# Performance work log

Measured on AMD Instinct MI355X. Metric: run time of the kernel, lower is better.

Reference implementation:

```python
import jax, jax.numpy as jnp
import numpy as np

THRESH = 0.3

def _quantize_ternary(s):
    # straight-through ternary: forward value is q, gradient is identity
    q = jnp.where(s > THRESH, 1.0, jnp.where(s < -THRESH, -1.0, 0.0))
    return s + jax.lax.stop_gradient(q - s)

def setup_inputs() -> dict:
    key = jax.random.key(0)
    k1, k2, k3 = jax.random.split(key, 3)
    B, D, T, C = 32768, 1024, 16, 1000
    x = jax.random.normal(k1, (B, D), dtype=jnp.float32)
    sigs_raw = jax.random.normal(k2, (T, D), dtype=jnp.float32) * 0.5
    # per-tile Linear(d_model, n_classes): weight [C, D], bias [C]
    W = jax.random.normal(k3, (T, C, D), dtype=jnp.float32) / np.sqrt(D)
    b = jnp.zeros((T, C), dtype=jnp.float32)
    return {"x": x, "sigs_raw": sigs_raw, "W": W, "b": b}

def reference(x, sigs_raw, W, b):
    sigs = _quantize_ternary(sigs_raw)          # [T, D] ternary values
    scores = x @ sigs.T                          # [B, T]
    tile_indices = jnp.argmax(scores, axis=-1)   # [B] top-1 routing
    n_tiles = W.shape[0]
    logits = jnp.zeros((x.shape[0], W.shape[1]), dtype=x.dtype)  # [B, C]
    # static loop over tiles: masked per-expert linear, combined by select
    for t in range(n_tiles):
        m = (tile_indices == t)[:, None]         # [B, 1]
        yt = x @ W[t].T + b[t]                   # [B, C]
        logits = jnp.where(m, yt, logits)
    return logits, tile_indices
```

## Files before the change

kernel.cpp:

```cpp
#include <hip/hip_runtime.h>

#define NBROWS 32768
#define ND 1024
#define NT 16
#define NC 1000
#define NHB 128
#define MAX_RB128 272

typedef short short8 __attribute__((ext_vector_type(8)));
typedef float f32x4 __attribute__((ext_vector_type(4)));
typedef unsigned short ushort_t;

typedef __attribute__((address_space(1))) const unsigned int* gas_t;
typedef __attribute__((address_space(3))) unsigned int* las_t;

__device__ __forceinline__ void async_copy16(const void* g, void* l) {
  __builtin_amdgcn_global_load_lds((gas_t)g, (las_t)l, 16, 0, 0);
}

__device__ __forceinline__ unsigned f2bf(float f) {
  unsigned u = __float_as_uint(f);
  u += 0x7FFFu + ((u >> 16) & 1u);
  return u >> 16;
}
__device__ __forceinline__ unsigned pk2(float a, float b) {
  return f2bf(a) | (f2bf(b) << 16);
}
__device__ __forceinline__ int swz(int row) { return (row & 3) ^ ((row >> 2) & 3); }

__global__ __launch_bounds__(512) void fused_pre(
    const float* __restrict__ x, const float* __restrict__ sigs_raw,
    int* __restrict__ tidx, float* __restrict__ out_idx,
    const float* __restrict__ W, ushort_t* __restrict__ wbf,
    ushort_t* __restrict__ xbf) {
  __shared__ signed char s_lds[NT * ND];
  int tid = threadIdx.x;
  int bid = blockIdx.x;
  if (bid >= 4096) {
    if (!wbf) return;
    size_t e = (((size_t)(bid - 4096)) * 512 + tid) * 8;
    int t = (int)(e >> 20);
    int rem = (int)(e & 1048575);
    int col = rem >> 10, k = rem & 1023;
    uint4 o;
    if (col < NC) {
      const float* src = W + ((size_t)t * NC + col) * ND + k;
      float4 a = *(const float4*)src;
      float4 b = *(const float4*)(src + 4);
      o = make_uint4(pk2(a.x, a.y), pk2(a.z, a.w), pk2(b.x, b.y), pk2(b.z, b.w));
    } else {
      o = make_uint4(0, 0, 0, 0);
    }
    *(uint4*)(wbf + e) = o;
    return;
  }
  for (int i = tid; i < NT * ND; i += 512) {
    float s = sigs_raw[i];
    s_lds[i] = (s > 0.3f) ? 1 : ((s < -0.3f) ? -1 : 0);
  }
  __syncthreads();
  int lane = tid & 63;
  int row = bid * 8 + (tid >> 6);
  const float* xr = x + (size_t)row * ND + lane * 16;
  float4 v0 = *(const float4*)(xr);
  float4 v1 = *(const float4*)(xr + 4);
  float4 v2 = *(const float4*)(xr + 8);
  float4 v3 = *(const float4*)(xr + 12);
  float xv[16] = {v0.x, v0.y, v0.z, v0.w, v1.x, v1.y, v1.z, v1.w,
                  v2.x, v2.y, v2.z, v2.w, v3.x, v3.y, v3.z, v3.w};
  if (xbf) {
    ushort_t* xo = xbf + (size_t)row * ND + lane * 16;
    *(uint4*)(xo) = make_uint4(pk2(v0.x, v0.y), pk2(v0.z, v0.w), pk2(v1.x, v1.y), pk2(v1.z, v1.w));
    *(uint4*)(xo + 8) = make_uint4(pk2(v2.x, v2.y), pk2(v2.z, v2.w), pk2(v3.x, v3.y), pk2(v3.z, v3.w));
  }
  float best = 0.0f;
  int bt = 0;
#pragma unroll
  for (int t = 0; t < NT; t++) {
    int4 sc = *(const int4*)(s_lds + t * ND + lane * 16);
    int wa[4] = {sc.x, sc.y, sc.z, sc.w};
    float p = 0.0f;
#pragma unroll
    for (int wi = 0; wi < 4; wi++)
#pragma unroll
      for (int bi = 0; bi < 4; bi++)
        p = fmaf((float)(signed char)(wa[wi] >> (8 * bi)), xv[wi * 4 + bi], p);
#pragma unroll
    for (int o = 32; o > 0; o >>= 1) p += __shfl_xor(p, o);
    if (t == 0 || p > best) { best = p; bt = t; }
  }
  if (lane == 0) {
    tidx[row] = bt;
    out_idx[row] = (float)bt;
  }
}

__global__ __launch_bounds__(256) void trix_hist(const int* __restrict__ tidx,
                                                 int* __restrict__ blkhist) {
  __shared__ int h[NT];
  int tid = threadIdx.x;
  if (tid < NT) h[tid] = 0;
  __syncthreads();
  int t = tidx[blockIdx.x * 256 + tid];
  atomicAdd(&h[t], 1);
  __syncthreads();
  if (tid < NT) blkhist[blockIdx.x * NT + tid] = h[tid];
}

__global__ __launch_bounds__(256) void trix_prefix(const int* __restrict__ blkhist,
                                                   int* __restrict__ blkbase,
                                                   int* __restrict__ meta) {
  __shared__ int part[NT][16];
  int tid = threadIdx.x;
  int t = tid >> 4, g = tid & 15;
  int s = 0;
  for (int b = g; b < NHB; b += 16) s += blkhist[b * NT + t];
  part[t][g] = s;
  __syncthreads();
  if (tid == 0) {
    int off = 0, cb2 = 0;
    for (int tt = 0; tt < NT; tt++) {
      int c = 0;
#pragma unroll
      for (int gg = 0; gg < 16; gg++) c += part[tt][gg];
      meta[tt] = c;
      meta[16 + tt] = off;
      meta[50 + tt] = cb2;
      off += c;
      cb2 += (c + 127) >> 7;
    }
    meta[32] = off;
    meta[66] = cb2;
  }
  __syncthreads();
  if (tid < NT) {
    int run = meta[16 + tid];
    for (int b = 0; b < NHB; b++) {
      blkbase[b * NT + tid] = run;
      run += blkhist[b * NT + tid];
    }
  }
}

__global__ __launch_bounds__(256) void trix_scatter(const int* __restrict__ tidx,
                                                    const int* __restrict__ blkbase,
                                                    int* __restrict__ rowlist) {
  __shared__ int h[NT];
  int tid = threadIdx.x;
  if (tid < NT) h[tid] = 0;
  __syncthreads();
  int row = blockIdx.x * 256 + tid;
  int t = tidx[row];
  int r = atomicAdd(&h[t], 1);
  rowlist[blkbase[blockIdx.x * NT + t] + r] = row;
}

__global__ __launch_bounds__(256, 3) void trix_gemm6(
    const ushort_t* __restrict__ xbf, const ushort_t* __restrict__ wbf,
    const float* __restrict__ bias, const int* __restrict__ meta,
    const int* __restrict__ rowlist, float* __restrict__ out) {
  __shared__ __align__(16) ushort_t A_lds[128 * 64];
  __shared__ __align__(16) ushort_t B_lds[128 * 64];
  __shared__ int rl[128];
  int bid = blockIdx.x;
  int w = (bid & 7) * 272 + (bid >> 3);
  int nb = w & 7, rb = w >> 3;
  if (rb >= meta[66]) return;
  int t = 0;
  while (t < NT - 1 && rb >= meta[51 + t]) t++;
  int row0 = meta[16 + t] + (rb - meta[50 + t]) * 128;
  int cnt = meta[17 + t] - row0;
  if (cnt > 128) cnt = 128;
  int tid = threadIdx.x;
  if (tid < 128) rl[tid] = rowlist[(tid < cnt) ? (row0 + tid) : row0];
  __syncthreads();

  int lane = tid & 63, wv = tid >> 6;
  int srow = lane >> 3;
  int schunk = ((lane & 7) ^ srow) * 8;
  const ushort_t* aS[4];
  const ushort_t* bS[4];
#pragma unroll
  for (int j = 0; j < 4; j++) {
    aS[j] = xbf + (size_t)rl[wv * 32 + j * 8 + srow] * ND + schunk;
    bS[j] = wbf + ((size_t)t << 20) + (size_t)(nb * 128 + wv * 32 + j * 8 + srow) * ND + schunk;
  }
  int ldst = wv * 2048 + lane * 8;

  int wr = wv >> 1, wc = wv & 1;
  int rsel = lane & 15, ksl = lane >> 4, rx = rsel & 7;
  int sl0 = (ksl ^ rx) * 8;
  int sl1 = ((4 + ksl) ^ rx) * 8;
  int aoff = (wr * 64 + rsel) * 64;
  int boff = (wc * 64 + rsel) * 64;

  f32x4 acc[4][4] = {};

#pragma unroll 1
  for (int k0 = 0; k0 < ND; k0 += 64) {
#pragma unroll
    for (int j = 0; j < 4; j++) {
      async_copy16(aS[j] + k0, &A_lds[ldst + j * 512]);
      async_copy16(bS[j] + k0, &B_lds[ldst + j * 512]);
    }
    __syncthreads();
    short8 af[4][2], bf2[2][2];
#pragma unroll
    for (int m = 0; m < 4; m++) {
      af[m][0] = *(const short8*)(&A_lds[aoff + m * 1024 + sl0]);
      af[m][1] = *(const short8*)(&A_lds[aoff + m * 1024 + sl1]);
    }
#pragma unroll
    for (int nh = 0; nh < 2; nh++) {
#pragma unroll
      for (int j = 0; j < 2; j++) {
        int n = nh * 2 + j;
        bf2[j][0] = *(const short8*)(&B_lds[boff + n * 1024 + sl0]);
        bf2[j][1] = *(const short8*)(&B_lds[boff + n * 1024 + sl1]);
      }
#pragma unroll
      for (int m = 0; m < 4; m++)
#pragma unroll
        for (int j = 0; j < 2; j++) {
          acc[m][nh * 2 + j] = __builtin_amdgcn_mfma_f32_16x16x32_bf16(
              af[m][0], bf2[j][0], acc[m][nh * 2 + j], 0, 0, 0);
          acc[m][nh * 2 + j] = __builtin_amdgcn_mfma_f32_16x16x32_bf16(
              af[m][1], bf2[j][1], acc[m][nh * 2 + j], 0, 0, 0);
        }
    }
    __syncthreads();
  }

  float bv[4];
  int bcol[4];
#pragma unroll
  for (int n = 0; n < 4; ++n) {
    bcol[n] = nb * 128 + wc * 64 + n * 16 + rsel;
    bv[n] = (bcol[n] < NC) ? bias[t * NC + bcol[n]] : 0.0f;
  }
#pragma unroll
  for (int m = 0; m < 4; ++m) {
#pragma unroll
    for (int r = 0; r < 4; ++r) {
      int lr = wr * 64 + m * 16 + ksl * 4 + r;
      if (lr < cnt) {
        size_t ob = (size_t)rl[lr] * NC;
#pragma unroll
        for (int n = 0; n < 4; ++n)
          if (bcol[n] < NC) out[ob + bcol[n]] = acc[m][n][r] + bv[n];
      }
    }
  }
}

__global__ __launch_bounds__(256) void trix_gemm_fb(
    const float* __restrict__ x, const float* __restrict__ W,
    const float* __restrict__ bias, const int* __restrict__ meta,
    const int* __restrict__ rowlist, float* __restrict__ out) {
  __shared__ __align__(16) unsigned char aT[128 * 64];
  __shared__ __align__(16) unsigned char bT[128 * 64];
  __shared__ int rl[128];
  int nb = blockIdx.x, rb = blockIdx.y;
  if (rb >= meta[66]) return;
  int t = 0;
  while (t < NT - 1 && rb >= meta[51 + t]) t++;
  int row0 = meta[16 + t] + (rb - meta[50 + t]) * 128;
  int cnt = meta[17 + t] - row0;
  if (cnt > 128) cnt = 128;
  int tid = threadIdx.x;
  if (tid < 128) rl[tid] = rowlist[(tid < cnt) ? (row0 + tid) : row0];
  __syncthreads();
  int half = tid & 1, rloc = tid >> 1;
  const float* xp = x + (size_t)rl[rloc] * ND + half * 16;
  int wn = nb * 128 + rloc;
  if (wn > NC - 1) wn = NC - 1;
  const float* wp = W + ((size_t)t * NC + wn) * ND + half * 16;
  int sw = swz(rloc);
  unsigned char* aw0 = aT + rloc * 64 + (((half * 2 + 0) ^ sw) << 4);
  unsigned char* aw1 = aT + rloc * 64 + (((half * 2 + 1) ^ sw) << 4);
  unsigned char* bw0 = bT + rloc * 64 + (((half * 2 + 0) ^ sw) << 4);
  unsigned char* bw1 = bT + rloc * 64 + (((half * 2 + 1) ^ sw) << 4);
  int lane = tid & 63, wv = tid >> 6;
  int wr = wv >> 1, wc = wv & 1;
  int rsel = lane & 15, slot = lane >> 4;
  f32x4 acc[4][4] = {};
  for (int k0 = 0; k0 < ND; k0 += 32) {
    const float* xk = xp + k0;
    const float* wk = wp + k0;
    float4 a0 = *(const float4*)(xk);
    float4 a1 = *(const float4*)(xk + 4);
    float4 a2 = *(const float4*)(xk + 8);
    float4 a3 = *(const float4*)(xk + 12);
    float4 b0 = *(const float4*)(wk);
    float4 b1 = *(const float4*)(wk + 4);
    float4 b2 = *(const float4*)(wk + 8);
    float4 b3 = *(const float4*)(wk + 12);
    *(uint4*)aw0 = make_uint4(pk2(a0.x, a0.y), pk2(a0.z, a0.w), pk2(a1.x, a1.y), pk2(a1.z, a1.w));
    *(uint4*)aw1 = make_uint4(pk2(a2.x, a2.y), pk2(a2.z, a2.w), pk2(a3.x, a3.y), pk2(a3.z, a3.w));
    *(uint4*)bw0 = make_uint4(pk2(b0.x, b0.y), pk2(b0.z, b0.w), pk2(b1.x, b1.y), pk2(b1.z, b1.w));
    *(uint4*)bw1 = make_uint4(pk2(b2.x, b2.y), pk2(b2.z, b2.w), pk2(b3.x, b3.y), pk2(b3.z, b3.w));
    __syncthreads();
    short8 af2[4], bfr[4];
#pragma unroll
    for (int i = 0; i < 4; i++) {
      int arr = wr * 64 + i * 16 + rsel;
      af2[i] = *(const short8*)(aT + arr * 64 + ((slot ^ swz(arr)) << 4));
      int brr = wc * 64 + i * 16 + rsel;
      bfr[i] = *(const short8*)(bT + brr * 64 + ((slot ^ swz(brr)) << 4));
    }
#pragma unroll
    for (int mi = 0; mi < 4; mi++)
#pragma unroll
      for (int ni = 0; ni < 4; ni++)
        acc[mi][ni] = __builtin_amdgcn_mfma_f32_16x16x32_bf16(af2[mi], bfr[ni], acc[mi][ni], 0, 0, 0);
    __syncthreads();
  }
#pragma unroll
  for (int mi = 0; mi < 4; mi++) {
#pragma unroll
    for (int r = 0; r < 4; r++) {
      int rloc2 = wr * 64 + mi * 16 + slot * 4 + r;
      if (rloc2 < cnt) {
        size_t obase = (size_t)rl[rloc2] * NC;
#pragma unroll
        for (int ni = 0; ni < 4; ni++) {
          int col = nb * 128 + wc * 64 + ni * 16 + rsel;
          if (col < NC) out[obase + col] = acc[mi][ni][r] + bias[t * NC + col];
        }
      }
    }
  }
}

extern "C" void kernel_launch(void* const* d_in, const int* in_sizes, int n_in,
                              void* d_out, int out_size, void* d_ws, size_t ws_size,
                              hipStream_t stream) {
  const float* x = (const float*)d_in[0];
  const float* sigs = (const float*)d_in[1];
  const float* W = (const float*)d_in[2];
  const float* bias = (const float*)d_in[3];
  float* out = (float*)d_out;

  const size_t XBF_B = (size_t)NBROWS * ND * 2;
  const size_t WBF_B = (size_t)NT * 1024 * ND * 2;
  bool fast = ws_size >= XBF_B + WBF_B + (1 << 20);

  char* wsb = (char*)d_ws;
  ushort_t* xbf = nullptr;
  ushort_t* wbf = nullptr;
  int* tidx;
  if (fast) {
    xbf = (ushort_t*)wsb;
    wbf = (ushort_t*)(wsb + XBF_B);
    tidx = (int*)(wsb + XBF_B + WBF_B);
  } else {
    tidx = (int*)wsb;
  }
  int* rowlist = tidx + NBROWS;
  int* meta = rowlist + NBROWS;
  int* blkhist = meta + 80;
  int* blkbase = blkhist + NHB * NT;

  fused_pre<<<8192, 512, 0, stream>>>(x, sigs, tidx, out + (size_t)NBROWS * NC, W, wbf, xbf);
  trix_hist<<<NHB, 256, 0, stream>>>(tidx, blkhist);
  trix_prefix<<<1, 256, 0, stream>>>(blkhist, blkbase, meta);
  trix_scatter<<<NHB, 256, 0, stream>>>(tidx, blkbase, rowlist);
  if (fast) {
    trix_gemm6<<<8 * MAX_RB128, 256, 0, stream>>>(xbf, wbf, bias, meta, rowlist, out);
  } else {
    trix_gemm_fb<<<dim3(8, MAX_RB128), 256, 0, stream>>>(x, W, bias, meta, rowlist, out);
  }
}
```

Measured before the change: 179.7 us.

## Overlap next K-tile global-to-LDS copy with MFMA compute in grouped GEMM

```diff
diff --git a/kernel.cpp b/kernel.cpp
--- a/kernel.cpp
+++ b/kernel.cpp
@@ -155,7 +155,7 @@
   rowlist[blkbase[blockIdx.x * NT + t] + r] = row;
 }
 
-__global__ __launch_bounds__(256, 3) void trix_gemm6(
+__global__ __launch_bounds__(256, 3) void trix_gemm7(
     const ushort_t* __restrict__ xbf, const ushort_t* __restrict__ wbf,
     const float* __restrict__ bias, const int* __restrict__ meta,
     const int* __restrict__ rowlist, float* __restrict__ out) {
@@ -196,40 +196,46 @@
 
   f32x4 acc[4][4] = {};
 
+#define STAGE(KTL)                                            \
+  _Pragma("unroll") for (int j = 0; j < 4; j++) {             \
+    async_copy16(aS[j] + (KTL) * 64, &A_lds[ldst + j * 512]); \
+    async_copy16(bS[j] + (KTL) * 64, &B_lds[ldst + j * 512]); \
+  }
+
+  STAGE(0);
+  asm volatile("s_waitcnt vmcnt(0)" ::: "memory");
+  __builtin_amdgcn_s_barrier();
+
 #pragma unroll 1
-  for (int k0 = 0; k0 < ND; k0 += 64) {
-#pragma unroll
-    for (int j = 0; j < 4; j++) {
-      async_copy16(aS[j] + k0, &A_lds[ldst + j * 512]);
-      async_copy16(bS[j] + k0, &B_lds[ldst + j * 512]);
-    }
-    __syncthreads();
-    short8 af[4][2], bf2[2][2];
+  for (int kt = 0; kt < 16; ++kt) {
+    short8 af[4][2], bf2[4][2];
 #pragma unroll
     for (int m = 0; m < 4; m++) {
       af[m][0] = *(const short8*)(&A_lds[aoff + m * 1024 + sl0]);
       af[m][1] = *(const short8*)(&A_lds[aoff + m * 1024 + sl1]);
     }
 #pragma unroll
-    for (int nh = 0; nh < 2; nh++) {
-#pragma unroll
-      for (int j = 0; j < 2; j++) {
-        int n = nh * 2 + j;
-        bf2[j][0] = *(const short8*)(&B_lds[boff + n * 1024 + sl0]);
-        bf2[j][1] = *(const short8*)(&B_lds[boff + n * 1024 + sl1]);
+    for (int n = 0; n < 4; n++) {
+      bf2[n][0] = *(const short8*)(&B_lds[boff + n * 1024 + sl0]);
+      bf2[n][1] = *(const short8*)(&B_lds[boff + n * 1024 + sl1]);
+    }
+    asm volatile("s_waitcnt lgkmcnt(0)" ::: "memory");
+    __builtin_amdgcn_sched_barrier(0);
+    __builtin_amdgcn_s_barrier();
+    if (kt < 15) STAGE(kt + 1);
+    __builtin_amdgcn_s_setprio(1);
+#pragma unroll
+    for (int n = 0; n < 4; n++)
+#pragma unroll
+      for (int m = 0; m < 4; m++) {
+        acc[m][n] = __builtin_amdgcn_mfma_f32_16x16x32_bf16(af[m][0], bf2[n][0], acc[m][n], 0, 0, 0);
+        acc[m][n] = __builtin_amdgcn_mfma_f32_16x16x32_bf16(af[m][1], bf2[n][1], acc[m][n], 0, 0, 0);
       }
-#pragma unroll
-      for (int m = 0; m < 4; m++)
-#pragma unroll
-        for (int j = 0; j < 2; j++) {
-          acc[m][nh * 2 + j] = __builtin_amdgcn_mfma_f32_16x16x32_bf16(
-              af[m][0], bf2[j][0], acc[m][nh * 2 + j], 0, 0, 0);
-          acc[m][nh * 2 + j] = __builtin_amdgcn_mfma_f32_16x16x32_bf16(
-              af[m][1], bf2[j][1], acc[m][nh * 2 + j], 0, 0, 0);
-        }
-    }
-    __syncthreads();
-  }
+    __builtin_amdgcn_s_setprio(0);
+    asm volatile("s_waitcnt vmcnt(0)" ::: "memory");
+    __builtin_amdgcn_s_barrier();
+  }
+#undef STAGE
 
   float bv[4];
   int bcol[4];
@@ -366,7 +372,7 @@
   trix_prefix<<<1, 256, 0, stream>>>(blkhist, blkbase, meta);
   trix_scatter<<<NHB, 256, 0, stream>>>(tidx, blkbase, rowlist);
   if (fast) {
-    trix_gemm6<<<8 * MAX_RB128, 256, 0, stream>>>(xbf, wbf, bias, meta, rowlist, out);
+    trix_gemm7<<<8 * MAX_RB128, 256, 0, stream>>>(xbf, wbf, bias, meta, rowlist, out);
   } else {
     trix_gemm_fb<<<dim3(8, MAX_RB128), 256, 0, stream>>>(x, W, bias, meta, rowlist, out);
   }
```

Result: no change. 176.3 us (-1.9%).
